# Kernel tuning notes

Hardware: AMD Instinct MI355X
Metric: run time of the kernel (lower is better)

Reference implementation:

```python
import jax, jax.numpy as jnp
import numpy as np

NEG_SLOPE = 0.01  # torch nn.LeakyReLU default


def setup_inputs() -> dict:
    key = jax.random.key(0)
    k1, k2, k3, k4, k5 = jax.random.split(key, 5)
    B, C, N, O = 32, 512, 1024, 512
    x = jax.random.normal(k1, (B, C, N), dtype=jnp.float32)
    wq = jax.random.normal(k2, (C,), dtype=jnp.float32) * (1.0 / np.sqrt(C))
    wk = jax.random.normal(k3, (C,), dtype=jnp.float32) * (1.0 / np.sqrt(C))
    wm = jax.random.normal(k4, (O, C), dtype=jnp.float32) * (1.0 / np.sqrt(C))
    bm = jax.random.normal(k5, (O,), dtype=jnp.float32) * 0.01
    return {"x": x, "wq": wq, "wk": wk, "wm": wm, "bm": bm}


def reference(x, wq, wk, wm, bm):
    # x: [B, C, N]
    q = jnp.einsum('c,bcn->bn', wq, x)            # [B, N] (Conv1d C->1, k=1, no bias)
    k = jnp.einsum('c,bcn->bn', wk, x)            # [B, N]
    scores = q[:, None, :] + k[:, :, None]        # [B, N, N] additive broadcast
    scores = jnp.where(scores > 0, scores, NEG_SLOPE * scores)  # LeakyReLU
    att = jax.nn.softmax(scores, axis=-1)         # softmax over last dim
    agg = jnp.einsum('bcn,bmn->bcm', x, att)      # weighted aggregation [B, C, N]
    out = jnp.einsum('oc,bcm->bom', wm, agg) + bm[None, :, None]  # Conv1d k=1
    return jax.nn.relu(out)
```

## Files before the change

kernel.cpp:

```cpp
#include <hip/hip_runtime.h>


constexpr int B = 32, C = 512, N = 1024, O = 512;
constexpr float L2E = 1.4426950408889634f;

typedef _Float16 half8 __attribute__((ext_vector_type(8)));
typedef _Float16 half4v __attribute__((ext_vector_type(4)));
typedef _Float16 half2v __attribute__((ext_vector_type(2)));
typedef float f32x4 __attribute__((ext_vector_type(4)));
typedef float f32x16 __attribute__((ext_vector_type(16)));

#if __has_builtin(__builtin_amdgcn_exp2f)
#define EXP2(x) __builtin_amdgcn_exp2f(x)
#else
#define EXP2(x) exp2f(x)
#endif

__device__ __forceinline__ half8 cvt8(float4 a, float4 b) {
  half8 h;
  h[0] = (_Float16)a.x; h[1] = (_Float16)a.y; h[2] = (_Float16)a.z; h[3] = (_Float16)a.w;
  h[4] = (_Float16)b.x; h[5] = (_Float16)b.y; h[6] = (_Float16)b.z; h[7] = (_Float16)b.w;
  return h;
}

__device__ __forceinline__ unsigned fenc(float x) {
  unsigned u = __float_as_uint(x);
  return (u & 0x80000000u) ? ~u : (u ^ 0x80000000u);
}
__device__ __forceinline__ float fdec(unsigned e) {
  unsigned u = (e & 0x80000000u) ? (e ^ 0x80000000u) : ~e;
  return __uint_as_float(u);
}

__device__ __forceinline__ void gload16(const _Float16* g, _Float16* l) {
  __builtin_amdgcn_global_load_lds(
      (const __attribute__((address_space(1))) unsigned int*)(g),
      (__attribute__((address_space(3))) unsigned int*)(l), 16, 0, 0);
}

__global__ __launch_bounds__(256) void wmh_kernel(const float* __restrict__ wm,
                                                  _Float16* __restrict__ wmh,
                                                  unsigned* __restrict__ qmax_u) {
  int i = (blockIdx.x * 256 + threadIdx.x) * 8;
  float4 a = *(const float4*)(wm + i);
  float4 b = *(const float4*)(wm + i + 4);
  *(half8*)(wmh + i) = cvt8(a, b);
  if (blockIdx.x == 0 && threadIdx.x < 64) qmax_u[threadIdx.x] = 0u;
}

__global__ __launch_bounds__(256) void prep_kernel(const float* __restrict__ x,
    const float* __restrict__ wq, const float* __restrict__ wk,
    float* __restrict__ q, float* __restrict__ k, unsigned* __restrict__ qmax_u,
    _Float16* __restrict__ xhT) {
  __shared__ half2v Ts[32 * 67];
  int b  = blockIdx.y;
  int n0 = blockIdx.x * 64;
  int t = threadIdx.x;
  int cp = t >> 3;
  int ng = t & 7;
  const float* xbase = x + ((size_t)b * C + 2 * cp) * N + n0 + ng * 8;
  int nl = t >> 2;
  int hq = t & 3;
  _Float16* xout = xhT + ((size_t)b * N + n0 + nl) * C + hq * 16;
  float aq[8] = {}, ak[8] = {};

  for (int ch = 0; ch < 8; ++ch) {
    int c0 = ch * 64;
    const float* xr = xbase + (size_t)c0 * N;
    float4 a0 = *(const float4*)(xr);
    float4 a1 = *(const float4*)(xr + 4);
    float4 b0 = *(const float4*)(xr + N);
    float4 b1 = *(const float4*)(xr + N + 4);
    float2 wq2 = *(const float2*)&wq[c0 + 2 * cp];
    float2 wk2 = *(const float2*)&wk[c0 + 2 * cp];
    aq[0] = fmaf(wq2.x, a0.x, fmaf(wq2.y, b0.x, aq[0]));
    aq[1] = fmaf(wq2.x, a0.y, fmaf(wq2.y, b0.y, aq[1]));
    aq[2] = fmaf(wq2.x, a0.z, fmaf(wq2.y, b0.z, aq[2]));
    aq[3] = fmaf(wq2.x, a0.w, fmaf(wq2.y, b0.w, aq[3]));
    aq[4] = fmaf(wq2.x, a1.x, fmaf(wq2.y, b1.x, aq[4]));
    aq[5] = fmaf(wq2.x, a1.y, fmaf(wq2.y, b1.y, aq[5]));
    aq[6] = fmaf(wq2.x, a1.z, fmaf(wq2.y, b1.z, aq[6]));
    aq[7] = fmaf(wq2.x, a1.w, fmaf(wq2.y, b1.w, aq[7]));
    ak[0] = fmaf(wk2.x, a0.x, fmaf(wk2.y, b0.x, ak[0]));
    ak[1] = fmaf(wk2.x, a0.y, fmaf(wk2.y, b0.y, ak[1]));
    ak[2] = fmaf(wk2.x, a0.z, fmaf(wk2.y, b0.z, ak[2]));
    ak[3] = fmaf(wk2.x, a0.w, fmaf(wk2.y, b0.w, ak[3]));
    ak[4] = fmaf(wk2.x, a1.x, fmaf(wk2.y, b1.x, ak[4]));
    ak[5] = fmaf(wk2.x, a1.y, fmaf(wk2.y, b1.y, ak[5]));
    ak[6] = fmaf(wk2.x, a1.z, fmaf(wk2.y, b1.z, ak[6]));
    ak[7] = fmaf(wk2.x, a1.w, fmaf(wk2.y, b1.w, ak[7]));
    {
      half2v* xp = &Ts[cp * 67 + ng * 8];
      xp[0] = half2v{(_Float16)a0.x, (_Float16)b0.x};
      xp[1] = half2v{(_Float16)a0.y, (_Float16)b0.y};
      xp[2] = half2v{(_Float16)a0.z, (_Float16)b0.z};
      xp[3] = half2v{(_Float16)a0.w, (_Float16)b0.w};
      xp[4] = half2v{(_Float16)a1.x, (_Float16)b1.x};
      xp[5] = half2v{(_Float16)a1.y, (_Float16)b1.y};
      xp[6] = half2v{(_Float16)a1.z, (_Float16)b1.z};
      xp[7] = half2v{(_Float16)a1.w, (_Float16)b1.w};
    }
    __syncthreads();
    half8 o0h, o1h;
#pragma unroll
    for (int u = 0; u < 4; ++u) {
      half2v pr = Ts[(hq * 8 + u) * 67 + nl];
      o0h[2 * u] = pr[0]; o0h[2 * u + 1] = pr[1];
    }
#pragma unroll
    for (int u = 4; u < 8; ++u) {
      half2v pr = Ts[(hq * 8 + u) * 67 + nl];
      o1h[2 * (u - 4)] = pr[0]; o1h[2 * (u - 4) + 1] = pr[1];
    }
    *(half8*)(xout + c0)     = o0h;
    *(half8*)(xout + c0 + 8) = o1h;
    __syncthreads();
  }

  float* red = (float*)Ts;
#pragma unroll
  for (int j = 0; j < 8; ++j) red[cp * 67 + ng * 8 + j] = aq[j];
  __syncthreads();
  float qv = -1e30f;
  if (t < 64) {
    float s = 0.f;
#pragma unroll
    for (int p = 0; p < 32; ++p) s += red[p * 67 + t];
    qv = L2E * s;
    q[b * N + n0 + t] = qv;
  }
  __syncthreads();
#pragma unroll
  for (int j = 0; j < 8; ++j) red[cp * 67 + ng * 8 + j] = ak[j];
  __syncthreads();
  if (t < 64) {
    float s = 0.f;
#pragma unroll
    for (int p = 0; p < 32; ++p) s += red[p * 67 + t];
    k[b * N + n0 + t] = L2E * s;
    float m = qv;
#pragma unroll
    for (int off = 32; off > 0; off >>= 1) m = fmaxf(m, __shfl_down(m, off, 64));
    if (t == 0) atomicMax(&qmax_u[b], fenc(m));
  }
}

__global__ __launch_bounds__(256) void gemm_y_kernel(const _Float16* __restrict__ xhT,
    const _Float16* __restrict__ wmh, _Float16* __restrict__ Yt) {
  __shared__ __align__(16) _Float16 As[2][128 * 32];
  int f = blockIdx.x;
  int xcd = f & 7, g = f >> 3;
  int o_id = g & 3;
  int p2 = xcd * 32 + (g >> 2);
  int n_id = p2 & 7, b = p2 >> 3;
  int n0 = n_id * 128, o0 = o_id * 128;
  int t = threadIdx.x;
  int w = t >> 6, l = t & 63;
  int nw = w >> 1, ow = w & 1;
  int lm = l & 15, q8 = (l >> 4) * 8, q4 = (l >> 4) * 4;

  const _Float16* asrc[2];
#pragma unroll
  for (int m = 0; m < 2; ++m) {
    int u = m * 256 + t;
    asrc[m] = xhT + ((size_t)b * N + n0 + (u >> 2)) * C + (u & 3) * 8;
  }
  const _Float16* wb[4];
#pragma unroll
  for (int j = 0; j < 4; ++j)
    wb[j] = wmh + (size_t)(o0 + ow * 64 + j * 16 + lm) * C + q8;

#pragma unroll
  for (int m = 0; m < 2; ++m)
    gload16(asrc[m], &As[0][(m * 256 + (t & ~63)) * 8]);
  __syncthreads();

  f32x4 acc[4][4] = {};
  for (int it = 0; it < 16; ++it) {
    int p = it & 1;
    if (it < 15) {
      int c1 = (it + 1) * 32;
#pragma unroll
      for (int m = 0; m < 2; ++m)
        gload16(asrc[m] + c1, &As[p ^ 1][(m * 256 + (t & ~63)) * 8]);
    }
    int c0 = it * 32;
    half8 bf[4];
#pragma unroll
    for (int j = 0; j < 4; ++j) bf[j] = *(const half8*)(wb[j] + c0);
#pragma unroll
    for (int i = 0; i < 4; ++i) {
      half8 af = *(const half8*)&As[p][(nw * 64 + i * 16 + lm) * 32 + q8];
#pragma unroll
      for (int j = 0; j < 4; ++j)
        acc[i][j] = __builtin_amdgcn_mfma_f32_16x16x32_f16(af, bf[j], acc[i][j], 0, 0, 0);
    }
    __syncthreads();
  }

#pragma unroll
  for (int i = 0; i < 4; ++i) {
    int n_b = n0 + nw * 64 + i * 16 + q4;
#pragma unroll
    for (int j = 0; j < 4; ++j) {
      int o_c = o0 + ow * 64 + j * 16 + lm;
      half4v h;
      h[0] = (_Float16)acc[i][j][0];
      h[1] = (_Float16)acc[i][j][1];
      h[2] = (_Float16)acc[i][j][2];
      h[3] = (_Float16)acc[i][j][3];
      *(half4v*)&Yt[((size_t)b * O + o_c) * N + n_b] = h;
    }
  }
}

__global__ __launch_bounds__(512) void gemm_out_kernel(const _Float16* __restrict__ Yt,
    const float* __restrict__ q, const float* __restrict__ k,
    const unsigned* __restrict__ qmax_u, const float* __restrict__ bm,
    float* __restrict__ out) {
  __shared__ __align__(16) float qs[N];
  __shared__ __align__(16) _Float16 Ys[2][256 * 40];
  __shared__ float izs[256];
  int b  = blockIdx.y;
  int o0 = blockIdx.x * 256;
  int m0 = blockIdx.z * 256;
  int t = threadIdx.x;
  int w = t >> 6, l = t & 63;
  int ml = l & 31, g2 = l >> 5;

  *(float2*)&qs[t * 2] = *(const float2*)&q[b * N + t * 2];

  float qmv = fdec(qmax_u[b]);
  float km = k[b * N + m0 + w * 32 + ml];
  float s0 = qmv + km;
  float M  = fmaxf(s0, 0.01f * s0);
  float kc2 = km - M;
  float kc3 = fmaf(0.01f, km, -M);

  half8 ones;
#pragma unroll
  for (int jj = 0; jj < 8; ++jj) ones[jj] = (_Float16)1.0f;
  f32x16 acc_z = {};
  int yr = t >> 1, yp = t & 1;
  const _Float16* ysrc = Yt + ((size_t)b * O + o0 + yr) * N + yp * 16;

  {
    half8 z0 = *(const half8*)(ysrc);
    half8 z1 = *(const half8*)(ysrc + 8);
    *(half8*)&Ys[0][yr * 40 + yp * 16]     = z0;
    *(half8*)&Ys[0][yr * 40 + yp * 16 + 8] = z1;
  }
  __syncthreads();

  f32x16 acc[8] = {};
  for (int it = 0; it < N / 32; ++it) {
    int p = it & 1;
    int n0k = it * 32;
    half8 z0, z1;
    if (it < N / 32 - 1) {
      z0 = *(const half8*)(ysrc + n0k + 32);
      z1 = *(const half8*)(ysrc + n0k + 40);
    }
#pragma unroll
    for (int kh = 0; kh < 2; ++kh) {
      float4 qa = *(const float4*)&qs[n0k + kh * 16 + g2 * 8];
      float4 qb = *(const float4*)&qs[n0k + kh * 16 + g2 * 8 + 4];
      float qv[8] = {qa.x, qa.y, qa.z, qa.w, qb.x, qb.y, qb.z, qb.w};
      half8 af;
#pragma unroll
      for (int jj = 0; jj < 8; ++jj) {
        float arg = fmaxf(qv[jj] + kc2, fmaf(0.01f, qv[jj], kc3));
        af[jj] = (_Float16)EXP2(arg);
      }
      acc_z = __builtin_amdgcn_mfma_f32_32x32x16_f16(af, ones, acc_z, 0, 0, 0);
#pragma unroll
      for (int s = 0; s < 8; ++s) {
        half8 bf = *(const half8*)&Ys[p][(s * 32 + ml) * 40 + kh * 16 + g2 * 8];
        acc[s] = __builtin_amdgcn_mfma_f32_32x32x16_f16(af, bf, acc[s], 0, 0, 0);
      }
    }
    if (it < N / 32 - 1) {
      *(half8*)&Ys[p ^ 1][yr * 40 + yp * 16]     = z0;
      *(half8*)&Ys[p ^ 1][yr * 40 + yp * 16 + 8] = z1;
    }
    __syncthreads();
  }

  if (ml == 0) {
#pragma unroll
    for (int rq = 0; rq < 4; ++rq)
#pragma unroll
      for (int r = 0; r < 4; ++r)
        izs[w * 32 + r + 8 * rq + 4 * g2] = 1.0f / acc_z[rq * 4 + r];
  }
  __syncthreads();

  float4 izv[4];
#pragma unroll
  for (int rq = 0; rq < 4; ++rq)
    izv[rq] = *(const float4*)&izs[w * 32 + 8 * rq + 4 * g2];

#pragma unroll
  for (int s = 0; s < 8; ++s) {
    int o_c = o0 + s * 32 + ml;
    float bias = bm[o_c];
#pragma unroll
    for (int rq = 0; rq < 4; ++rq) {
      int m_b = m0 + w * 32 + 8 * rq + 4 * g2;
      float4 r;
      r.x = fmaxf(fmaf(acc[s][rq * 4 + 0], izv[rq].x, bias), 0.f);
      r.y = fmaxf(fmaf(acc[s][rq * 4 + 1], izv[rq].y, bias), 0.f);
      r.z = fmaxf(fmaf(acc[s][rq * 4 + 2], izv[rq].z, bias), 0.f);
      r.w = fmaxf(fmaf(acc[s][rq * 4 + 3], izv[rq].w, bias), 0.f);
      *(float4*)&out[((size_t)b * O + o_c) * N + m_b] = r;
    }
  }
}

extern "C" void kernel_launch(void* const* d_in, const int* in_sizes, int n_in,
                              void* d_out, int out_size, void* d_ws, size_t ws_size,
                              hipStream_t stream) {
  const float* x  = (const float*)d_in[0];
  const float* wq = (const float*)d_in[1];
  const float* wk = (const float*)d_in[2];
  const float* wm = (const float*)d_in[3];
  const float* bm = (const float*)d_in[4];
  float* out = (float*)d_out;

  float* q    = (float*)d_ws;
  float* k    = q + B * N;
  unsigned* qmax_u = (unsigned*)(k + B * N);
  _Float16* wmh = (_Float16*)(qmax_u + 64);
  _Float16* Yt  = wmh + (size_t)O * C;
  _Float16* xhT = (_Float16*)d_out;

  wmh_kernel<<<dim3(O * C / (256 * 8)), 256, 0, stream>>>(wm, wmh, qmax_u);
  prep_kernel<<<dim3(N / 64, B), 256, 0, stream>>>(x, wq, wk, q, k, qmax_u, xhT);
  gemm_y_kernel<<<dim3(1024), 256, 0, stream>>>(xhT, wmh, Yt);
  gemm_out_kernel<<<dim3(O / 256, B, N / 256), 512, 0, stream>>>(Yt, q, k, qmax_u, bm, out);
}
```

Measured before the change: 214.8 us.

## Factor softmax exponent into per-row and per-column exps, drop LDS staging of Y

Rewrites gemm_out so the attention weight exp(leaky(q+k)-M) is computed as max(exp(q)*exp(k-M), exp(0.01q)*exp(0.01k-M)) from precomputed half-precision factors, replacing per-element exp2 with packed half multiplies and max. Swaps the MFMA roles so each wave loads its Y operand straight from global memory into registers with a one-step prefetch, removing the LDS double buffer and per-iteration barriers. The row sum is now computed by wave 0 with fdot2 instead of an extra MFMA against ones. It also remaps the grid to a 1D XCD-aware block order and sets launch bounds of 2 blocks per SM. The risks are fp16 overflow or underflow in exp(q), and wave 0 carrying extra reduction work.

```diff
diff --git a/kernel.cpp b/kernel.cpp
--- a/kernel.cpp
+++ b/kernel.cpp
@@ -36,6 +36,20 @@
   __builtin_amdgcn_global_load_lds(
       (const __attribute__((address_space(1))) unsigned int*)(g),
       (__attribute__((address_space(3))) unsigned int*)(l), 16, 0, 0);
+}
+
+__device__ __forceinline__ float dot8z(half8 a, float c) {
+#if __has_builtin(__builtin_amdgcn_fdot2)
+  half2v one2; one2[0] = (_Float16)1.0f; one2[1] = (_Float16)1.0f;
+  c = __builtin_amdgcn_fdot2(__builtin_shufflevector(a, a, 0, 1), one2, c, false);
+  c = __builtin_amdgcn_fdot2(__builtin_shufflevector(a, a, 2, 3), one2, c, false);
+  c = __builtin_amdgcn_fdot2(__builtin_shufflevector(a, a, 4, 5), one2, c, false);
+  c = __builtin_amdgcn_fdot2(__builtin_shufflevector(a, a, 6, 7), one2, c, false);
+#else
+#pragma unroll
+  for (int j = 0; j < 8; ++j) c += (float)a[j];
+#endif
+  return c;
 }
 
 __global__ __launch_bounds__(256) void wmh_kernel(const float* __restrict__ wm,
@@ -214,105 +228,102 @@
   }
 }
 
-__global__ __launch_bounds__(512) void gemm_out_kernel(const _Float16* __restrict__ Yt,
+__global__ __launch_bounds__(512, 2) void gemm_out_kernel(const _Float16* __restrict__ Yt,
     const float* __restrict__ q, const float* __restrict__ k,
     const unsigned* __restrict__ qmax_u, const float* __restrict__ bm,
     float* __restrict__ out) {
-  __shared__ __align__(16) float qs[N];
-  __shared__ __align__(16) _Float16 Ys[2][256 * 40];
+  __shared__ __align__(16) _Float16 us[N];
+  __shared__ __align__(16) _Float16 vs[N];
   __shared__ float izs[256];
-  int b  = blockIdx.y;
-  int o0 = blockIdx.x * 256;
-  int m0 = blockIdx.z * 256;
+  int f = blockIdx.x;
+  int xcd = f & 7, g = f >> 3;
+  int m_id = g & 3;
+  int pair = xcd * 8 + (g >> 2);
+  int o_id = pair & 1, b = pair >> 1;
+  int o0 = o_id * 256, m0 = m_id * 256;
   int t = threadIdx.x;
   int w = t >> 6, l = t & 63;
   int ml = l & 31, g2 = l >> 5;
 
-  *(float2*)&qs[t * 2] = *(const float2*)&q[b * N + t * 2];
-
+  {
+    float2 q2 = *(const float2*)&q[b * N + t * 2];
+    us[t * 2]     = (_Float16)EXP2(q2.x);
+    us[t * 2 + 1] = (_Float16)EXP2(q2.y);
+    vs[t * 2]     = (_Float16)EXP2(0.01f * q2.x);
+    vs[t * 2 + 1] = (_Float16)EXP2(0.01f * q2.y);
+  }
   float qmv = fdec(qmax_u[b]);
-  float km = k[b * N + m0 + w * 32 + ml];
-  float s0 = qmv + km;
-  float M  = fmaxf(s0, 0.01f * s0);
-  float kc2 = km - M;
-  float kc3 = fmaf(0.01f, km, -M);
-
-  half8 ones;
-#pragma unroll
-  for (int jj = 0; jj < 8; ++jj) ones[jj] = (_Float16)1.0f;
-  f32x16 acc_z = {};
-  int yr = t >> 1, yp = t & 1;
-  const _Float16* ysrc = Yt + ((size_t)b * O + o0 + yr) * N + yp * 16;
-
-  {
-    half8 z0 = *(const half8*)(ysrc);
-    half8 z1 = *(const half8*)(ysrc + 8);
-    *(half8*)&Ys[0][yr * 40 + yp * 16]     = z0;
-    *(half8*)&Ys[0][yr * 40 + yp * 16 + 8] = z1;
-  }
+  _Float16 am[8], bmh[8];
+#pragma unroll
+  for (int s = 0; s < 8; ++s) {
+    float km = k[b * N + m0 + s * 32 + ml];
+    float s0 = qmv + km;
+    float M = fmaxf(s0, 0.01f * s0);
+    am[s]  = (_Float16)EXP2(km - M);
+    bmh[s] = (_Float16)EXP2(fmaf(0.01f, km, -M));
+  }
+  const _Float16* ysrc = Yt + ((size_t)b * O + o0 + w * 32 + ml) * N + g2 * 8;
   __syncthreads();
 
   f32x16 acc[8] = {};
+  float z8[8] = {};
+  half8 bf0 = *(const half8*)(ysrc);
+  half8 bf1 = *(const half8*)(ysrc + 16);
+#pragma unroll 2
   for (int it = 0; it < N / 32; ++it) {
-    int p = it & 1;
     int n0k = it * 32;
-    half8 z0, z1;
+    half8 nb0, nb1;
     if (it < N / 32 - 1) {
-      z0 = *(const half8*)(ysrc + n0k + 32);
-      z1 = *(const half8*)(ysrc + n0k + 40);
-    }
-#pragma unroll
-    for (int kh = 0; kh < 2; ++kh) {
-      float4 qa = *(const float4*)&qs[n0k + kh * 16 + g2 * 8];
-      float4 qb = *(const float4*)&qs[n0k + kh * 16 + g2 * 8 + 4];
-      float qv[8] = {qa.x, qa.y, qa.z, qa.w, qb.x, qb.y, qb.z, qb.w};
-      half8 af;
-#pragma unroll
-      for (int jj = 0; jj < 8; ++jj) {
-        float arg = fmaxf(qv[jj] + kc2, fmaf(0.01f, qv[jj], kc3));
-        af[jj] = (_Float16)EXP2(arg);
+      nb0 = *(const half8*)(ysrc + n0k + 32);
+      nb1 = *(const half8*)(ysrc + n0k + 48);
+    }
+    {
+      half8 u8 = *(const half8*)&us[n0k + g2 * 8];
+      half8 v8 = *(const half8*)&vs[n0k + g2 * 8];
+#pragma unroll
+      for (int s = 0; s < 8; ++s) {
+        half8 af = __builtin_elementwise_max(u8 * am[s], v8 * bmh[s]);
+        if (w == 0) z8[s] = dot8z(af, z8[s]);
+        acc[s] = __builtin_amdgcn_mfma_f32_32x32x16_f16(af, bf0, acc[s], 0, 0, 0);
       }
-      acc_z = __builtin_amdgcn_mfma_f32_32x32x16_f16(af, ones, acc_z, 0, 0, 0);
+    }
+    {
+      half8 u8 = *(const half8*)&us[n0k + 16 + g2 * 8];
+      half8 v8 = *(const half8*)&vs[n0k + 16 + g2 * 8];
 #pragma unroll
       for (int s = 0; s < 8; ++s) {
-        half8 bf = *(const half8*)&Ys[p][(s * 32 + ml) * 40 + kh * 16 + g2 * 8];
-        acc[s] = __builtin_amdgcn_mfma_f32_32x32x16_f16(af, bf, acc[s], 0, 0, 0);
+        half8 af = __builtin_elementwise_max(u8 * am[s], v8 * bmh[s]);
+        if (w == 0) z8[s] = dot8z(af, z8[s]);
+        acc[s] = __builtin_amdgcn_mfma_f32_32x32x16_f16(af, bf1, acc[s], 0, 0, 0);
       }
     }
-    if (it < N / 32 - 1) {
-      *(half8*)&Ys[p ^ 1][yr * 40 + yp * 16]     = z0;
-      *(half8*)&Ys[p ^ 1][yr * 40 + yp * 16 + 8] = z1;
-    }
-    __syncthreads();
-  }
-
-  if (ml == 0) {
-#pragma unroll
-    for (int rq = 0; rq < 4; ++rq)
-#pragma unroll
-      for (int r = 0; r < 4; ++r)
-        izs[w * 32 + r + 8 * rq + 4 * g2] = 1.0f / acc_z[rq * 4 + r];
-  }
-  __syncthreads();
-
-  float4 izv[4];
-#pragma unroll
-  for (int rq = 0; rq < 4; ++rq)
-    izv[rq] = *(const float4*)&izs[w * 32 + 8 * rq + 4 * g2];
-
+    bf0 = nb0; bf1 = nb1;
+  }
+
+  if (w == 0) {
+#pragma unroll
+    for (int s = 0; s < 8; ++s) {
+      float zt = z8[s] + __shfl_xor(z8[s], 32, 64);
+      if (l < 32) izs[s * 32 + l] = 1.0f / zt;
+    }
+  }
+  __syncthreads();
+
+  int o_c = o0 + w * 32 + ml;
+  float bias = bm[o_c];
+  float* orow = out + ((size_t)b * O + o_c) * N + m0;
 #pragma unroll
   for (int s = 0; s < 8; ++s) {
-    int o_c = o0 + s * 32 + ml;
-    float bias = bm[o_c];
 #pragma unroll
     for (int rq = 0; rq < 4; ++rq) {
-      int m_b = m0 + w * 32 + 8 * rq + 4 * g2;
+      float4 izv = *(const float4*)&izs[s * 32 + 8 * rq + 4 * g2];
+      int m_b = s * 32 + 8 * rq + 4 * g2;
       float4 r;
-      r.x = fmaxf(fmaf(acc[s][rq * 4 + 0], izv[rq].x, bias), 0.f);
-      r.y = fmaxf(fmaf(acc[s][rq * 4 + 1], izv[rq].y, bias), 0.f);
-      r.z = fmaxf(fmaf(acc[s][rq * 4 + 2], izv[rq].z, bias), 0.f);
-      r.w = fmaxf(fmaf(acc[s][rq * 4 + 3], izv[rq].w, bias), 0.f);
-      *(float4*)&out[((size_t)b * O + o_c) * N + m_b] = r;
+      r.x = fmaxf(fmaf(acc[s][rq * 4 + 0], izv.x, bias), 0.f);
+      r.y = fmaxf(fmaf(acc[s][rq * 4 + 1], izv.y, bias), 0.f);
+      r.z = fmaxf(fmaf(acc[s][rq * 4 + 2], izv.z, bias), 0.f);
+      r.w = fmaxf(fmaf(acc[s][rq * 4 + 3], izv.w, bias), 0.f);
+      *(float4*)&orow[m_b] = r;
     }
   }
 }
@@ -337,5 +348,5 @@
   wmh_kernel<<<dim3(O * C / (256 * 8)), 256, 0, stream>>>(wm, wmh, qmax_u);
   prep_kernel<<<dim3(N / 64, B), 256, 0, stream>>>(x, wq, wk, q, k, qmax_u, xhT);
   gemm_y_kernel<<<dim3(1024), 256, 0, stream>>>(xhT, wmh, Yt);
-  gemm_out_kernel<<<dim3(O / 256, B, N / 256), 512, 0, stream>>>(Yt, q, k, qmax_u, bm, out);
-}
+  gemm_out_kernel<<<dim3(256), 512, 0, stream>>>(Yt, q, k, qmax_u, bm, out);
+}
```

Measured after the change: 722.2 us. 236% more time.
